# Kernel optimization log

Hardware: AMD Instinct MI355X
Metric: run time of the kernel (lower is better)

## Reference

```python
import jax, jax.numpy as jnp
import numpy as np

NB, HD, NL, NF = 5, 64, 4, 10           # num_bins, hidden_dim(d_model), num_layers, num_frames
DI, DS, DC, DTR = 128, 16, 4, 4          # d_inner=2*HD, d_state, d_conv, dt_rank=ceil(HD/16)
B, H, W = 4, 64, 64


def _conv2d(x, w, b):
    y = jax.lax.conv_general_dilated(x, w, (1, 1), 'SAME',
                                     dimension_numbers=('NCHW', 'OIHW', 'NCHW'))
    return y + b[None, :, None, None]


def _bn_relu(x, gamma, beta, eps=1e-5):
    # BatchNorm2d in training mode: biased batch stats over (N,H,W)
    mean = x.mean(axis=(0, 2, 3), keepdims=True)
    var = x.var(axis=(0, 2, 3), keepdims=True)
    y = (x - mean) * jax.lax.rsqrt(var + eps)
    return jax.nn.relu(y * gamma[None, :, None, None] + beta[None, :, None, None])


def _silu(x):
    return x * jax.nn.sigmoid(x)


def _causal_dwconv(x, w, b):
    # x: (B,L,DI), w: (DI,K) depthwise causal conv, b: (DI,)
    K = w.shape[1]
    L = x.shape[1]
    xp = jnp.pad(x, ((0, 0), (K - 1, 0), (0, 0)))
    y = sum(xp[:, k:k + L, :] * w[:, k] for k in range(K))
    return y + b


def _selective_scan(u, delta, A, Bm, Cm, D):
    # u,delta: (B,L,DI); A: (DI,DS); Bm,Cm: (B,L,DS); D: (DI,)
    dT, BT, CT, uT = (t.transpose(1, 0, 2) for t in (delta, Bm, Cm, u))
    h0 = jnp.zeros((u.shape[0], A.shape[0], A.shape[1]), u.dtype)

    def step(h, inp):
        d_t, B_t, C_t, u_t = inp                     # (B,DI),(B,DS),(B,DS),(B,DI)
        dA = jnp.exp(d_t[:, :, None] * A)            # (B,DI,DS)
        h = dA * h + (d_t * u_t)[:, :, None] * B_t[:, None, :]
        y = jnp.einsum('bds,bs->bd', h, C_t)
        return h, y

    _, ys = jax.lax.scan(step, h0, (dT, BT, CT, uT))  # ys: (L,B,DI)
    return ys.transpose(1, 0, 2) + u * D


def _mamba(x, in_proj, conv_w, conv_b, x_proj, dt_w, dt_b, A_log, Dp, out_proj):
    xz = x @ in_proj.T                               # (B,L,2*DI)
    xi, z = jnp.split(xz, 2, axis=-1)
    xi = _silu(_causal_dwconv(xi, conv_w, conv_b))
    xdbc = xi @ x_proj.T                             # (B,L,DTR+2*DS)
    dt, Bm, Cm = jnp.split(xdbc, [DTR, DTR + DS], axis=-1)
    delta = jax.nn.softplus(dt @ dt_w.T + dt_b)
    A = -jnp.exp(A_log)
    y = _selective_scan(xi, delta, A, Bm, Cm, Dp)
    return (y * _silu(z)) @ out_proj.T


def setup_inputs() -> dict:
    key = jax.random.key(0)
    ks = jax.random.split(key, 20)
    s = 0.02
    inp = {
        'x': jax.random.normal(ks[0], (B, NB, H, W), jnp.float32),
        'enc_w': jax.random.normal(ks[1], (HD, NB, 3, 3), jnp.float32) * s,
        'enc_b': jnp.zeros((HD,), jnp.float32),
        'enc_g': jnp.ones((HD,), jnp.float32),
        'enc_be': jnp.zeros((HD,), jnp.float32),
        'in_proj': jax.random.normal(ks[2], (NL, 2 * DI, HD), jnp.float32) * s,
        'conv_w': jax.random.normal(ks[3], (NL, DI, DC), jnp.float32) * s,
        'conv_b': jnp.zeros((NL, DI), jnp.float32),
        'x_proj': jax.random.normal(ks[4], (NL, DTR + 2 * DS, DI), jnp.float32) * s,
        'dt_w': jax.random.normal(ks[5], (NL, DI, DTR), jnp.float32) * s,
        'dt_b': jax.random.normal(ks[6], (NL, DI), jnp.float32) * 0.1 - 4.0,
        'A_log': jnp.broadcast_to(jnp.log(jnp.arange(1, DS + 1, dtype=jnp.float32)),
                                  (NL, DI, DS)).copy(),
        'Dp': jnp.ones((NL, DI), jnp.float32),
        'out_proj': jax.random.normal(ks[7], (NL, HD, DI), jnp.float32) * s,
        'dec1_w': jax.random.normal(ks[8], (HD, HD, 3, 3), jnp.float32) * s,
        'dec1_b': jnp.zeros((HD,), jnp.float32),
        'dec1_g': jnp.ones((HD,), jnp.float32),
        'dec1_be': jnp.zeros((HD,), jnp.float32),
        'dec2_w': jax.random.normal(ks[9], (NF, HD, 3, 3), jnp.float32) * s,
        'dec2_b': jnp.zeros((NF,), jnp.float32),
    }
    return inp


def reference(x, enc_w, enc_b, enc_g, enc_be, in_proj, conv_w, conv_b, x_proj,
              dt_w, dt_b, A_log, Dp, out_proj, dec1_w, dec1_b, dec1_g, dec1_be,
              dec2_w, dec2_b):
    Bb, _, Hh, Ww = x.shape
    h = _bn_relu(_conv2d(x, enc_w, enc_b), enc_g, enc_be)   # (B,HD,H,W)
    t = h.reshape(Bb, HD, Hh * Ww).transpose(0, 2, 1)        # (B,L,HD)
    for i in range(NL):
        t = t + _mamba(t, in_proj[i], conv_w[i], conv_b[i], x_proj[i],
                       dt_w[i], dt_b[i], A_log[i], Dp[i], out_proj[i])
    h = t.transpose(0, 2, 1).reshape(Bb, HD, Hh, Ww)
    h = _bn_relu(_conv2d(h, dec1_w, dec1_b), dec1_g, dec1_be)
    return _conv2d(h, dec2_w, dec2_b)                        # (B,NF,H,W)
```

## Files before the change

kernel.cpp:

```cpp
#include <hip/hip_runtime.h>
#include <hip/hip_bf16.h>

#define BB   4
#define NBC  5
#define HD   64
#define NLAYER 4
#define NFC  10
#define DIM  128
#define DSN  16
#define DCN  4
#define DTRK 4
#define HH   64
#define WWD  64
#define LL   4096
#define MM   (BB*LL)
#define NCHUNK 128
#define CLEN   32
#define TSTEP  16

__global__ void k_prep_all(const float* __restrict__ in_proj, const float* __restrict__ out_proj,
                           const float* __restrict__ dec1_w, const float* __restrict__ dec2_w,
                           float* __restrict__ wTin, float* __restrict__ wTout,
                           float* __restrict__ wT1, float* __restrict__ wT2,
                           float* __restrict__ stats, float* __restrict__ stats2) {
    int idx = blockIdx.x * blockDim.x + threadIdx.x;
    if (idx < 65536) {
        int n = idx & 255, k = (idx >> 8) & 63, l = idx >> 14;
        wTin[idx] = in_proj[(l << 14) + (n << 6) + k];
    } else if (idx < 98304) {
        int j = idx - 65536;
        int n = j & 63, k = (j >> 6) & 127, l = j >> 13;
        wTout[j] = out_proj[(l << 13) + (n << 7) + k];
    } else if (idx < 135168) {
        int j = idx - 98304;
        int co = j & 63, tap = (j >> 6) % 9, ci = j / 576;
        wT1[j] = dec1_w[co * 576 + ci * 9 + tap];
    } else if (idx < 142848) {
        int j = idx - 135168;
        int tap = j % 12, t2 = j / 12, co = t2 % NFC, ci = t2 / NFC;
        wT2[j] = (tap < 9) ? dec2_w[co * 576 + ci * 9 + tap] : 0.f;
    } else if (idx < 143104) {
        int j = idx - 142848;
        if (j < 128) stats[j] = 0.f; else stats2[j - 128] = 0.f;
    }
}

__global__ void k_enc_conv(const float* __restrict__ x, const float* __restrict__ w,
                           const float* __restrict__ bias, float* __restrict__ out,
                           float* __restrict__ stats) {
    __shared__ float r1[256], r2[256];
    int tid = threadIdx.x;
    int idx = blockIdx.x * 256 + tid;
    int wx = idx & 63;
    int hy = (idx >> 6) & 63;
    int co = (idx >> 12) & 63;
    int b  = idx >> 18;
    float acc = bias[co];
    for (int ci = 0; ci < NBC; ++ci) {
        const float* xin = x + (((long)(b * NBC + ci)) << 12);
        const float* wp  = w + (co * NBC + ci) * 9;
        #pragma unroll
        for (int kh = 0; kh < 3; ++kh) {
            int ih = hy + kh - 1;
            if (ih < 0 || ih >= HH) continue;
            #pragma unroll
            for (int kw = 0; kw < 3; ++kw) {
                int iw = wx + kw - 1;
                if (iw < 0 || iw >= WWD) continue;
                acc += xin[(ih << 6) + iw] * wp[kh * 3 + kw];
            }
        }
    }
    out[idx] = acc;
    r1[tid] = acc; r2[tid] = acc * acc;
    __syncthreads();
    for (int off = 128; off > 0; off >>= 1) {
        if (tid < off) { r1[tid] += r1[tid + off]; r2[tid] += r2[tid + off]; }
        __syncthreads();
    }
    if (tid == 0) {
        atomicAdd(&stats[co], r1[0]);
        atomicAdd(&stats[64 + co], r2[0]);
    }
}

__global__ __launch_bounds__(256, 1) void k_gemm_in_bn(const float* __restrict__ src,
                                                       const float* __restrict__ stats,
                                                       const float* __restrict__ g,
                                                       const float* __restrict__ be,
                                                       const float* __restrict__ wT,
                                                       float* __restrict__ tout,
                                                       float* __restrict__ xz) {
    __shared__ __align__(16) float ts[64 * 68];
    __shared__ float sc[64], sh[64];
    long m0 = (long)blockIdx.x << 6;
    int b = (int)(m0 >> 12);
    int hw0 = (int)(m0 & 4095);
    int tid = threadIdx.x;
    if (tid < 64) {
        float m = stats[tid] * (1.f / 16384.f);
        float var = stats[64 + tid] * (1.f / 16384.f) - m * m;
        float ss = g[tid] * rsqrtf(var + 1e-5f);
        sc[tid] = ss; sh[tid] = be[tid] - m * ss;
    }
    __syncthreads();
    for (int i = tid; i < 4096; i += 256) {
        int pix = i & 63, c = i >> 6;
        float v = src[(((long)((b << 6) + c)) << 12) + hw0 + pix];
        ts[pix * 68 + c] = fmaxf(v * sc[c] + sh[c], 0.f);
    }
    __syncthreads();
    for (int i = tid; i < 4096; i += 256) {
        int r = i >> 6, c = i & 63;
        tout[(m0 + r) * 64 + c] = ts[r * 68 + c];
    }
    int rg = tid >> 5;
    int cg = tid & 31;
    float acc[8][8] = {};
    int n0 = cg << 3;
    for (int k4 = 0; k4 < 16; ++k4) {
        float4 a[8];
        #pragma unroll
        for (int r2 = 0; r2 < 8; ++r2)
            a[r2] = *(const float4*)&ts[((rg << 3) + r2) * 68 + (k4 << 2)];
        #pragma unroll
        for (int kk = 0; kk < 4; ++kk) {
            const float* wr = wT + (((k4 << 2) + kk) << 8) + n0;
            float4 w0 = *(const float4*)&wr[0];
            float4 w1 = *(const float4*)&wr[4];
            #pragma unroll
            for (int r2 = 0; r2 < 8; ++r2) {
                float av = (kk == 0) ? a[r2].x : (kk == 1) ? a[r2].y
                         : (kk == 2) ? a[r2].z : a[r2].w;
                acc[r2][0] += av * w0.x; acc[r2][1] += av * w0.y;
                acc[r2][2] += av * w0.z; acc[r2][3] += av * w0.w;
                acc[r2][4] += av * w1.x; acc[r2][5] += av * w1.y;
                acc[r2][6] += av * w1.z; acc[r2][7] += av * w1.w;
            }
        }
    }
    #pragma unroll
    for (int r2 = 0; r2 < 8; ++r2) {
        long m = m0 + (rg << 3) + r2;
        *(float4*)&xz[(m << 8) + n0]     = make_float4(acc[r2][0], acc[r2][1], acc[r2][2], acc[r2][3]);
        *(float4*)&xz[(m << 8) + n0 + 4] = make_float4(acc[r2][4], acc[r2][5], acc[r2][6], acc[r2][7]);
    }
}

__global__ __launch_bounds__(256, 2) void k_xproj_fused(
        const float* __restrict__ xz, const float* __restrict__ cw,
        const float* __restrict__ cb, const float* __restrict__ Wx,
        const float* __restrict__ dw, const float* __restrict__ dbias,
        const float* __restrict__ A_log,
        float* __restrict__ xi, float* __restrict__ xdbc,
        float* __restrict__ delta, float* __restrict__ Pb, float* __restrict__ Sb) {
    __shared__ float xz_s[35 * 132];
    __shared__ float xi_s[32 * 132];
    __shared__ float w_s[36 * 132];
    __shared__ float xs[32 * 40];
    __shared__ float cwT[4 * 128];
    __shared__ float cb_s[128];
    long m0 = (long)blockIdx.x << 5;
    int l0 = (int)(m0 & 4095);
    int b = (int)(m0 >> 12);
    int chunk = l0 >> 5;
    int tid = threadIdx.x;

    for (int i = tid; i < 35 * 128; i += 256) {
        int j = i >> 7, k = i & 127;
        int l = l0 - 3 + j;
        float v = 0.f;
        if (l >= 0) v = xz[(m0 - 3 + j) * 256 + k];
        xz_s[j * 132 + k] = v;
    }
    if (tid < 128) cb_s[tid] = cb[tid];
    for (int i = tid; i < 512; i += 256) {
        int kk = i >> 7, di = i & 127;
        cwT[(kk << 7) + di] = cw[(di << 2) + kk];
    }
    for (int i = tid; i < 4608; i += 256) {
        int n = i >> 7, k = i & 127;
        w_s[n * 132 + k] = Wx[i];
    }
    __syncthreads();

    for (int ii = 0; ii < 4; ++ii) {
        int i = tid + (ii << 8);
        int r = i >> 5;
        int d4 = (i & 31) << 2;
        float4 a = *(const float4*)&cb_s[d4];
        #pragma unroll
        for (int kk = 0; kk < 4; ++kk) {
            float4 xv = *(const float4*)&xz_s[(r + kk) * 132 + d4];
            float4 wv = *(const float4*)&cwT[(kk << 7) + d4];
            a.x += xv.x * wv.x; a.y += xv.y * wv.y;
            a.z += xv.z * wv.z; a.w += xv.w * wv.w;
        }
        a.x = a.x / (1.f + __expf(-a.x));
        a.y = a.y / (1.f + __expf(-a.y));
        a.z = a.z / (1.f + __expf(-a.z));
        a.w = a.w / (1.f + __expf(-a.w));
        *(float4*)&xi_s[r * 132 + d4] = a;
        *(float4*)&xi[(m0 + r) * 128 + d4] = a;
    }
    __syncthreads();

    int n = tid & 63;
    int rg = tid >> 6;
    if (n < 36) {
        float acc[8] = {0,0,0,0,0,0,0,0};
        for (int k4 = 0; k4 < 32; ++k4) {
            float4 w4 = *(const float4*)&w_s[n * 132 + (k4 << 2)];
            #pragma unroll
            for (int r = 0; r < 8; ++r) {
                float4 a4 = *(const float4*)&xi_s[((rg << 3) + r) * 132 + (k4 << 2)];
                acc[r] += a4.x * w4.x + a4.y * w4.y + a4.z * w4.z + a4.w * w4.w;
            }
        }
        #pragma unroll
        for (int r = 0; r < 8; ++r) {
            int rr = (rg << 3) + r;
            xdbc[(m0 + rr) * 36 + n] = acc[r];
            xs[rr * 40 + n] = acc[r];
        }
    }
    __syncthreads();

    float* delta_s = xz_s;
    for (int i = tid; i < 4096; i += 256) {
        int r = i >> 7, di = i & 127;
        float v = dbias[di];
        float4 d4 = *(const float4*)&dw[di << 2];
        v += xs[r * 40 + 0] * d4.x + xs[r * 40 + 1] * d4.y
           + xs[r * 40 + 2] * d4.z + xs[r * 40 + 3] * d4.w;
        float sp = (v > 20.f) ? v : log1pf(expf(v));
        delta[(m0 + r) * 128 + di] = sp;
        delta_s[r * 132 + di] = sp;
    }
    __syncthreads();

    {
        int di = tid >> 1;
        int dso = (tid & 1) << 3;
        float4 al0 = *(const float4*)&A_log[(di << 4) + dso];
        float4 al1 = *(const float4*)&A_log[(di << 4) + dso + 4];
        float Av[8] = { -expf(al0.x), -expf(al0.y), -expf(al0.z), -expf(al0.w),
                        -expf(al1.x), -expf(al1.y), -expf(al1.z), -expf(al1.w) };
        float h[8] = {0,0,0,0,0,0,0,0};
        float P[8] = {1,1,1,1,1,1,1,1};
        #pragma unroll 4
        for (int i = 0; i < CLEN; ++i) {
            float d = delta_s[i * 132 + di];
            float u = xi_s[i * 132 + di];
            float du = d * u;
            float4 B0 = *(float4*)&xs[i * 40 + DTRK + dso];
            float4 B1 = *(float4*)&xs[i * 40 + DTRK + dso + 4];
            float a0 = __expf(d * Av[0]); h[0] = a0 * h[0] + du * B0.x; P[0] *= a0;
            float a1 = __expf(d * Av[1]); h[1] = a1 * h[1] + du * B0.y; P[1] *= a1;
            float a2 = __expf(d * Av[2]); h[2] = a2 * h[2] + du * B0.z; P[2] *= a2;
            float a3 = __expf(d * Av[3]); h[3] = a3 * h[3] + du * B0.w; P[3] *= a3;
            float a4 = __expf(d * Av[4]); h[4] = a4 * h[4] + du * B1.x; P[4] *= a4;
            float a5 = __expf(d * Av[5]); h[5] = a5 * h[5] + du * B1.y; P[5] *= a5;
            float a6 = __expf(d * Av[6]); h[6] = a6 * h[6] + du * B1.z; P[6] *= a6;
            float a7 = __expf(d * Av[7]); h[7] = a7 * h[7] + du * B1.w; P[7] *= a7;
        }
        long o = (((long)chunk * BB + b) << 11) + (di << 4) + dso;
        *(float4*)&Pb[o]     = make_float4(P[0], P[1], P[2], P[3]);
        *(float4*)&Pb[o + 4] = make_float4(P[4], P[5], P[6], P[7]);
        *(float4*)&Sb[o]     = make_float4(h[0], h[1], h[2], h[3]);
        *(float4*)&Sb[o + 4] = make_float4(h[4], h[5], h[6], h[7]);
    }
}

__global__ void k_scan_p2(float* Pb, const float* __restrict__ Sb) {
    int t = blockIdx.x * blockDim.x + threadIdx.x;
    int b = t >> 11;
    int s = t & 2047;
    float h = 0.f;
    for (int c = 0; c < NCHUNK; ++c) {
        long idx = (((long)c * BB + b) << 11) + s;
        float p = Pb[idx];
        float sv = Sb[idx];
        Pb[idx] = h;
        h = p * h + sv;
    }
}

__global__ __launch_bounds__(256, 1) void k_scan_p3_oi(
        const float* __restrict__ delta, const float* __restrict__ xi,
        const float* __restrict__ xdbc, const float* __restrict__ A_log,
        const float* __restrict__ Dp, const float* __restrict__ xz,
        const float* __restrict__ hin, const float* __restrict__ wTo,
        const float* __restrict__ wTi, float* __restrict__ tio,
        float* __restrict__ xz_out, int doB) {
    __shared__ __align__(16) float d_s[32 * 132];
    __shared__ __align__(16) float u_s[32 * 132];
    __shared__ __align__(16) float bc_s[32 * 36];
    __shared__ __align__(16) float t_s[32 * 68];
    int chunk = blockIdx.x, b = blockIdx.y;
    int tid = threadIdx.x;
    long t0 = ((long)b << 12) + (long)chunk * CLEN;

    for (int i = tid; i < 1024; i += 256) {
        int r = i >> 5, c4 = (i & 31) << 2;
        *(float4*)&d_s[r * 132 + c4] = *(const float4*)&delta[(t0 + r) * 128 + c4];
        *(float4*)&u_s[r * 132 + c4] = *(const float4*)&xi[(t0 + r) * 128 + c4];
    }
    {
        int r = tid >> 3, c4 = (tid & 7) << 2;
        *(float4*)&bc_s[r * 36 + c4] = *(const float4*)&xdbc[(t0 + r) * 36 + DTRK + c4];
    }

    int di = tid >> 1;
    int dso = (tid & 1) << 3;
    float4 al0 = *(const float4*)&A_log[(di << 4) + dso];
    float4 al1 = *(const float4*)&A_log[(di << 4) + dso + 4];
    float Av[8] = { -expf(al0.x), -expf(al0.y), -expf(al0.z), -expf(al0.w),
                    -expf(al1.x), -expf(al1.y), -expf(al1.z), -expf(al1.w) };
    float Dv = Dp[di];
    long o = (((long)chunk * BB + b) << 11) + (di << 4) + dso;
    float4 h0 = *(const float4*)&hin[o];
    float4 h1 = *(const float4*)&hin[o + 4];
    float h[8] = { h0.x, h0.y, h0.z, h0.w, h1.x, h1.y, h1.z, h1.w };
    __syncthreads();

    #pragma unroll 4
    for (int i = 0; i < CLEN; ++i) {
        float d = d_s[i * 132 + di];
        float u = u_s[i * 132 + di];
        float du = d * u;
        const float* bc = &bc_s[i * 36];
        float4 B0 = *(const float4*)&bc[dso];
        float4 B1 = *(const float4*)&bc[dso + 4];
        float4 C0 = *(const float4*)&bc[16 + dso];
        float4 C1 = *(const float4*)&bc[16 + dso + 4];
        float a0 = __expf(d * Av[0]); h[0] = a0 * h[0] + du * B0.x;
        float a1 = __expf(d * Av[1]); h[1] = a1 * h[1] + du * B0.y;
        float a2 = __expf(d * Av[2]); h[2] = a2 * h[2] + du * B0.z;
        float a3 = __expf(d * Av[3]); h[3] = a3 * h[3] + du * B0.w;
        float a4 = __expf(d * Av[4]); h[4] = a4 * h[4] + du * B1.x;
        float a5 = __expf(d * Av[5]); h[5] = a5 * h[5] + du * B1.y;
        float a6 = __expf(d * Av[6]); h[6] = a6 * h[6] + du * B1.z;
        float a7 = __expf(d * Av[7]); h[7] = a7 * h[7] + du * B1.w;
        float yp = h[0] * C0.x + h[1] * C0.y + h[2] * C0.z + h[3] * C0.w
                 + h[4] * C1.x + h[5] * C1.y + h[6] * C1.z + h[7] * C1.w;
        yp += __shfl_xor(yp, 1);
        if (dso == 0)
            u_s[i * 132 + di] = yp + u * Dv;
    }
    __syncthreads();

    for (int i = tid; i < 1024; i += 256) {
        int r = i >> 5, c4 = (i & 31) << 2;
        float4 y4 = *(float4*)&u_s[r * 132 + c4];
        float4 z4 = *(const float4*)&xz[((t0 + r) << 8) + DIM + c4];
        y4.x *= z4.x / (1.f + __expf(-z4.x));
        y4.y *= z4.y / (1.f + __expf(-z4.y));
        y4.z *= z4.z / (1.f + __expf(-z4.z));
        y4.w *= z4.w / (1.f + __expf(-z4.w));
        *(float4*)&u_s[r * 132 + c4] = y4;
    }
    __syncthreads();

    {
        int rg = tid >> 4, cg = tid & 15;
        int n0 = cg << 2;
        float acc[2][4] = {};
        for (int k4 = 0; k4 < 32; ++k4) {
            float4 a0 = *(const float4*)&u_s[(rg << 1) * 132 + (k4 << 2)];
            float4 a1 = *(const float4*)&u_s[((rg << 1) + 1) * 132 + (k4 << 2)];
            #pragma unroll
            for (int kk = 0; kk < 4; ++kk) {
                const float* wr = wTo + (((k4 << 2) + kk) << 6) + n0;
                float4 w0 = *(const float4*)&wr[0];
                float av0 = (kk == 0) ? a0.x : (kk == 1) ? a0.y : (kk == 2) ? a0.z : a0.w;
                float av1 = (kk == 0) ? a1.x : (kk == 1) ? a1.y : (kk == 2) ? a1.z : a1.w;
                acc[0][0] += av0 * w0.x; acc[0][1] += av0 * w0.y;
                acc[0][2] += av0 * w0.z; acc[0][3] += av0 * w0.w;
                acc[1][0] += av1 * w0.x; acc[1][1] += av1 * w0.y;
                acc[1][2] += av1 * w0.z; acc[1][3] += av1 * w0.w;
            }
        }
        #pragma unroll
        for (int r2 = 0; r2 < 2; ++r2) {
            long m = t0 + (rg << 1) + r2;
            float4 tv = *(const float4*)&tio[(m << 6) + n0];
            tv.x += acc[r2][0]; tv.y += acc[r2][1];
            tv.z += acc[r2][2]; tv.w += acc[r2][3];
            *(float4*)&tio[(m << 6) + n0] = tv;
            *(float4*)&t_s[((rg << 1) + r2) * 68 + n0] = tv;
        }
    }
    if (!doB) return;
    __syncthreads();

    {
        int rg = tid >> 5, cgn = tid & 31;
        int n0 = cgn << 3;
        float acc[4][8] = {};
        for (int k4 = 0; k4 < 16; ++k4) {
            float4 a[4];
            #pragma unroll
            for (int r2 = 0; r2 < 4; ++r2)
                a[r2] = *(const float4*)&t_s[((rg << 2) + r2) * 68 + (k4 << 2)];
            #pragma unroll
            for (int kk = 0; kk < 4; ++kk) {
                const float* wr = wTi + (((k4 << 2) + kk) << 8) + n0;
                float4 w0 = *(const float4*)&wr[0];
                float4 w1 = *(const float4*)&wr[4];
                #pragma unroll
                for (int r2 = 0; r2 < 4; ++r2) {
                    float av = (kk == 0) ? a[r2].x : (kk == 1) ? a[r2].y
                             : (kk == 2) ? a[r2].z : a[r2].w;
                    acc[r2][0] += av * w0.x; acc[r2][1] += av * w0.y;
                    acc[r2][2] += av * w0.z; acc[r2][3] += av * w0.w;
                    acc[r2][4] += av * w1.x; acc[r2][5] += av * w1.y;
                    acc[r2][6] += av * w1.z; acc[r2][7] += av * w1.w;
                }
            }
        }
        #pragma unroll
        for (int r2 = 0; r2 < 4; ++r2) {
            long m = t0 + (rg << 2) + r2;
            *(float4*)&xz_out[(m << 8) + n0]     = make_float4(acc[r2][0], acc[r2][1], acc[r2][2], acc[r2][3]);
            *(float4*)&xz_out[(m << 8) + n0 + 4] = make_float4(acc[r2][4], acc[r2][5], acc[r2][6], acc[r2][7]);
        }
    }
}

__global__ __launch_bounds__(256, 1) void k_dec1_new(const float* __restrict__ tin,
                                                     const float* __restrict__ wT,
                                                     const float* __restrict__ bias,
                                                     float* __restrict__ out,
                                                     float* __restrict__ stats2) {
    __shared__ __align__(16) float x_s[64 * 132];
    __shared__ __align__(16) float w_s[4 * 4608];
    int tile = blockIdx.x;
    int b = blockIdx.y;
    int ty0 = (tile >> 3) << 3;
    int tx0 = (tile & 7) << 3;
    int tid = threadIdx.x;
    int wv = tid >> 6;
    int lane = tid & 63;
    int r = lane >> 3;
    int cg = lane & 7;

    for (int i = tid; i < 6400; i += 256) {
        int pl = i >> 6;
        int c = i & 63;
        int py = pl / 10, px = pl - py * 10;
        int ih = ty0 + py - 1, iw = tx0 + px - 1;
        float v = 0.f;
        if (ih >= 0 && ih < HH && iw >= 0 && iw < WWD)
            v = tin[(((long)((b << 12) + (ih << 6) + iw)) << 6) + c];
        x_s[c * 132 + py * 12 + px] = v;
    }
    float* myw = &w_s[wv * 4608];
    const float* gw = wT + (wv * 16) * 576;
    float4 pref[18];
    #pragma unroll
    for (int i = 0; i < 18; ++i)
        pref[i] = *(const float4*)&gw[(i * 64 + lane) * 4];
    #pragma unroll
    for (int i = 0; i < 18; ++i)
        *(float4*)&myw[(i * 64 + lane) * 4] = pref[i];
    __syncthreads();

    float acc[8][8] = {};
    #pragma unroll
    for (int ch = 0; ch < 2; ++ch) {
        if (ch == 0) {
            const float* gw1 = wT + (wv * 16 + 8) * 576;
            #pragma unroll
            for (int i = 0; i < 18; ++i)
                pref[i] = *(const float4*)&gw1[(i * 64 + lane) * 4];
        }
        for (int cl = 0; cl < 8; ++cl) {
            int cib = wv * 16 + ch * 8 + cl;
            float xrow[3][10];
            #pragma unroll
            for (int kh = 0; kh < 3; ++kh) {
                const float* xr = &x_s[cib * 132 + (r + kh) * 12];
                float4 a0 = *(const float4*)&xr[0];
                float4 a1 = *(const float4*)&xr[4];
                float2 a2 = *(const float2*)&xr[8];
                xrow[kh][0] = a0.x; xrow[kh][1] = a0.y; xrow[kh][2] = a0.z; xrow[kh][3] = a0.w;
                xrow[kh][4] = a1.x; xrow[kh][5] = a1.y; xrow[kh][6] = a1.z; xrow[kh][7] = a1.w;
                xrow[kh][8] = a2.x; xrow[kh][9] = a2.y;
            }
            const float* wp = &myw[cl * 576];
            #pragma unroll
            for (int kh = 0; kh < 3; ++kh) {
                #pragma unroll
                for (int kw = 0; kw < 3; ++kw) {
                    const float* wp2 = wp + (kh * 3 + kw) * 64 + (cg << 3);
                    float4 wa = *(const float4*)&wp2[0];
                    float4 wb = *(const float4*)&wp2[4];
                    #pragma unroll
                    for (int j = 0; j < 8; ++j) {
                        float xv = xrow[kh][kw + j];
                        acc[j][0] += xv * wa.x; acc[j][1] += xv * wa.y;
                        acc[j][2] += xv * wa.z; acc[j][3] += xv * wa.w;
                        acc[j][4] += xv * wb.x; acc[j][5] += xv * wb.y;
                        acc[j][6] += xv * wb.z; acc[j][7] += xv * wb.w;
                    }
                }
            }
        }
        if (ch == 0) {
            #pragma unroll
            for (int i = 0; i < 18; ++i)
                *(float4*)&myw[(i * 64 + lane) * 4] = pref[i];
        }
    }

    #pragma unroll
    for (int j = 0; j < 8; ++j) {
        *(float4*)&myw[lane * 68 + (j << 3)]     = make_float4(acc[j][0], acc[j][1], acc[j][2], acc[j][3]);
        *(float4*)&myw[lane * 68 + (j << 3) + 4] = make_float4(acc[j][4], acc[j][5], acc[j][6], acc[j][7]);
    }
    __syncthreads();

    float bv = bias[lane];
    float ssum = 0.f, ssq = 0.f;
    #pragma unroll
    for (int pp = 0; pp < 16; ++pp) {
        int pr = (wv << 1) + (pp >> 3);
        int pc = pp & 7;
        int ol = (pr << 3) + (lane >> 3);
        int ix = (pc << 3) + (lane & 7);
        float s = w_s[ol * 68 + ix] + w_s[4608 + ol * 68 + ix]
                + w_s[9216 + ol * 68 + ix] + w_s[13824 + ol * 68 + ix] + bv;
        out[(((long)((b << 12) + ((ty0 + pr) << 6) + tx0 + pc)) << 6) + lane] = s;
        ssum += s; ssq += s * s;
    }
    float* red = x_s;
    red[(wv << 6) + lane] = ssum;
    red[256 + (wv << 6) + lane] = ssq;
    __syncthreads();
    if (tid < 64) {
        float a = red[tid] + red[64 + tid] + red[128 + tid] + red[192 + tid];
        float q = red[256 + tid] + red[320 + tid] + red[384 + tid] + red[448 + tid];
        atomicAdd(&stats2[tid], a);
        atomicAdd(&stats2[64 + tid], q);
    }
}

__global__ void k_dec2_fused(const float* __restrict__ src, const float* __restrict__ stats2,
                             const float* __restrict__ g, const float* __restrict__ be,
                             const float* __restrict__ wT, const float* __restrict__ bias,
                             float* __restrict__ out) {
    __shared__ float x_s[64 * 101];
    __shared__ float w_s[64 * NFC * 12];
    __shared__ float sc_s[64];
    __shared__ float sh_s[64];
    int tile = blockIdx.x;
    int b = blockIdx.y;
    int ty0 = (tile >> 3) << 3;
    int tx0 = (tile & 7) << 3;
    int tid = threadIdx.x;

    if (tid < 64) {
        float m = stats2[tid] * (1.f / 16384.f);
        float var = stats2[64 + tid] * (1.f / 16384.f) - m * m;
        float s = g[tid] * rsqrtf(var + 1e-5f);
        sc_s[tid] = s;
        sh_s[tid] = be[tid] - m * s;
    }
    for (int i = tid; i < 64 * NFC * 12; i += 256)
        w_s[i] = wT[i];
    __syncthreads();

    for (int i = tid; i < 6400; i += 256) {
        int pl = i >> 6;
        int c = i & 63;
        int py = pl / 10, px = pl - py * 10;
        int ih = ty0 + py - 1, iw = tx0 + px - 1;
        float v = 0.f;
        if (ih >= 0 && ih < HH && iw >= 0 && iw < WWD) {
            v = src[((long)((b << 12) + (ih << 6) + iw)) * 64 + c];
            v = fmaxf(v * sc_s[c] + sh_s[c], 0.f);
        }
        x_s[c * 101 + pl] = v;
    }
    __syncthreads();

    int px = tid & 63;
    int py = px >> 3, pxx = px & 7;
    int cog = tid >> 6;
    float acc[3] = {0.f, 0.f, 0.f};
    int nco = (cog < 2) ? 3 : 2;

    for (int ci = 0; ci < 64; ++ci) {
        const float* xr = &x_s[ci * 101 + py * 10 + pxx];
        float xv[9];
        #pragma unroll
        for (int kh = 0; kh < 3; ++kh)
            #pragma unroll
            for (int kw = 0; kw < 3; ++kw)
                xv[kh * 3 + kw] = xr[kh * 10 + kw];
        #pragma unroll
        for (int j = 0; j < 3; ++j) {
            if (j >= nco) break;
            int co = cog + (j << 2);
            const float* wp = &w_s[(ci * NFC + co) * 12];
            float4 w0 = *(const float4*)&wp[0];
            float4 w1 = *(const float4*)&wp[4];
            float  w8 = wp[8];
            acc[j] += xv[0] * w0.x + xv[1] * w0.y + xv[2] * w0.z + xv[3] * w0.w
                    + xv[4] * w1.x + xv[5] * w1.y + xv[6] * w1.z + xv[7] * w1.w
                    + xv[8] * w8;
        }
    }
    int hw = ((ty0 + py) << 6) + tx0 + pxx;
    #pragma unroll
    for (int j = 0; j < 3; ++j) {
        if (j >= nco) break;
        int co = cog + (j << 2);
        out[((long)(b * NFC + co) << 12) + hw] = acc[j] + bias[co];
    }
}

extern "C" void kernel_launch(void* const* d_in, const int* in_sizes, int n_in,
                              void* d_out, int out_size, void* d_ws, size_t ws_size,
                              hipStream_t stream) {
    const float* x       = (const float*)d_in[0];
    const float* enc_w   = (const float*)d_in[1];
    const float* enc_b   = (const float*)d_in[2];
    const float* enc_g   = (const float*)d_in[3];
    const float* enc_be  = (const float*)d_in[4];
    const float* in_proj = (const float*)d_in[5];
    const float* conv_w  = (const float*)d_in[6];
    const float* conv_b  = (const float*)d_in[7];
    const float* x_proj  = (const float*)d_in[8];
    const float* dt_w    = (const float*)d_in[9];
    const float* dt_b    = (const float*)d_in[10];
    const float* A_log   = (const float*)d_in[11];
    const float* Dp      = (const float*)d_in[12];
    const float* out_prj = (const float*)d_in[13];
    const float* dec1_w  = (const float*)d_in[14];
    const float* dec1_b  = (const float*)d_in[15];
    const float* dec1_g  = (const float*)d_in[16];
    const float* dec1_be = (const float*)d_in[17];
    const float* dec2_w  = (const float*)d_in[18];
    const float* dec2_b  = (const float*)d_in[19];
    float* out = (float*)d_out;

    float* ws = (float*)d_ws;
    size_t off = 0;
    float* conv_buf  = ws + off; off += 1048576;
    float* stats     = ws + off; off += 128;
    float* stats2    = ws + off; off += 128;
    float* wT1       = ws + off; off += 36864;
    float* wT2       = ws + off; off += 7680;
    float* wTin      = ws + off; off += 65536;
    float* wTout     = ws + off; off += 32768;
    float* t_buf     = ws + off; off += 1048576;
    float* xz_buf    = ws + off; off += 4194304;
    float* xi_buf    = ws + off; off += 2097152;
    float* xdbc_buf  = ws + off; off += 589824;
    float* delta_buf = ws + off; off += 2097152;
    float* Sb_buf    = ws + off; off += 1048576;
    (void)ws_size; (void)in_sizes; (void)n_in; (void)out_size;

    float* Pb = conv_buf;
    float* Sb = Sb_buf;

    k_prep_all<<<560, 256, 0, stream>>>(in_proj, out_prj, dec1_w, dec2_w,
                                        wTin, wTout, wT1, wT2, stats, stats2);

    k_enc_conv<<<4096, 256, 0, stream>>>(x, enc_w, enc_b, conv_buf, stats);

    k_gemm_in_bn<<<256, 256, 0, stream>>>(conv_buf, stats, enc_g, enc_be, wTin, t_buf, xz_buf);
    dim3 pg(NCHUNK, BB);
    for (int i = 0; i < NLAYER; ++i) {
        k_xproj_fused<<<512, 256, 0, stream>>>(xz_buf, conv_w + i * DIM * DCN,
                                               conv_b + i * DIM, x_proj + i * 36 * DIM,
                                               dt_w + i * DIM * DTRK, dt_b + i * DIM,
                                               A_log + i * DIM * DSN,
                                               xi_buf, xdbc_buf, delta_buf, Pb, Sb);
        k_scan_p2<<<32, 256, 0, stream>>>(Pb, Sb);
        int doB = (i < NLAYER - 1) ? 1 : 0;
        k_scan_p3_oi<<<pg, 256, 0, stream>>>(delta_buf, xi_buf, xdbc_buf,
                                             A_log + i * DIM * DSN, Dp + i * DIM,
                                             xz_buf, Pb, wTout + i * 8192,
                                             wTin + ((i + 1) & 3) * 16384,
                                             t_buf, xz_buf, doB);
    }

    dim3 dg1(64, BB);
    k_dec1_new<<<dg1, 256, 0, stream>>>(t_buf, wT1, dec1_b, conv_buf, stats2);
    k_dec2_fused<<<dg1, 256, 0, stream>>>(conv_buf, stats2, dec1_g, dec1_be, wT2, dec2_b, out);
}
```

Before: 489.8 us.

## Recompute delta in scan kernel instead of storing it to global memory

Stops writing the softplus delta tensor from the x-projection kernel and rebuilds it in the scan/out-proj kernel from the dt columns of xdbc. This removes a 2M-float global write and read per layer. The cost is extra exp/log1p work in the scan kernel. It also rebalances the x_proj mini-GEMM across 252 threads instead of 144 and aliases t_s onto d_s to cut LDS use.

```diff
diff --git a/kernel.cpp b/kernel.cpp
--- a/kernel.cpp
+++ b/kernel.cpp
@@ -16,7 +16,6 @@
 #define MM   (BB*LL)
 #define NCHUNK 128
 #define CLEN   32
-#define TSTEP  16
 
 __global__ void k_prep_all(const float* __restrict__ in_proj, const float* __restrict__ out_proj,
                            const float* __restrict__ dec1_w, const float* __restrict__ dec2_w,
@@ -153,7 +152,7 @@
         const float* __restrict__ dw, const float* __restrict__ dbias,
         const float* __restrict__ A_log,
         float* __restrict__ xi, float* __restrict__ xdbc,
-        float* __restrict__ delta, float* __restrict__ Pb, float* __restrict__ Sb) {
+        float* __restrict__ Pb, float* __restrict__ Sb) {
     __shared__ float xz_s[35 * 132];
     __shared__ float xi_s[32 * 132];
     __shared__ float w_s[36 * 132];
@@ -205,23 +204,31 @@
     }
     __syncthreads();
 
-    int n = tid & 63;
-    int rg = tid >> 6;
-    if (n < 36) {
-        float acc[8] = {0,0,0,0,0,0,0,0};
-        for (int k4 = 0; k4 < 32; ++k4) {
-            float4 w4 = *(const float4*)&w_s[n * 132 + (k4 << 2)];
-            #pragma unroll
-            for (int r = 0; r < 8; ++r) {
-                float4 a4 = *(const float4*)&xi_s[((rg << 3) + r) * 132 + (k4 << 2)];
-                acc[r] += a4.x * w4.x + a4.y * w4.y + a4.z * w4.z + a4.w * w4.w;
+    {
+        int g2 = tid / 36;
+        int n = tid - g2 * 36;
+        const int r0tab[8] = {0, 5, 10, 15, 20, 24, 28, 32};
+        if (g2 < 7) {
+            int rbeg = r0tab[g2];
+            int cnt = r0tab[g2 + 1] - rbeg;
+            float acc[5] = {0, 0, 0, 0, 0};
+            for (int k4 = 0; k4 < 32; ++k4) {
+                float4 w4 = *(const float4*)&w_s[n * 132 + (k4 << 2)];
+                #pragma unroll
+                for (int j = 0; j < 5; ++j) {
+                    int r = rbeg + j; r = (r > 31) ? 31 : r;
+                    float4 a4 = *(const float4*)&xi_s[r * 132 + (k4 << 2)];
+                    acc[j] += a4.x * w4.x + a4.y * w4.y + a4.z * w4.z + a4.w * w4.w;
+                }
             }
-        }
-        #pragma unroll
-        for (int r = 0; r < 8; ++r) {
-            int rr = (rg << 3) + r;
-            xdbc[(m0 + rr) * 36 + n] = acc[r];
-            xs[rr * 40 + n] = acc[r];
+            #pragma unroll
+            for (int j = 0; j < 5; ++j) {
+                if (j < cnt) {
+                    int r = rbeg + j;
+                    xdbc[(m0 + r) * 36 + n] = acc[j];
+                    xs[r * 40 + n] = acc[j];
+                }
+            }
         }
     }
     __syncthreads();
@@ -233,9 +240,7 @@
         float4 d4 = *(const float4*)&dw[di << 2];
         v += xs[r * 40 + 0] * d4.x + xs[r * 40 + 1] * d4.y
            + xs[r * 40 + 2] * d4.z + xs[r * 40 + 3] * d4.w;
-        float sp = (v > 20.f) ? v : log1pf(expf(v));
-        delta[(m0 + r) * 128 + di] = sp;
-        delta_s[r * 132 + di] = sp;
+        delta_s[r * 132 + di] = (v > 20.f) ? v : log1pf(expf(v));
     }
     __syncthreads();
 
@@ -287,28 +292,37 @@
 }
 
 __global__ __launch_bounds__(256, 1) void k_scan_p3_oi(
-        const float* __restrict__ delta, const float* __restrict__ xi,
-        const float* __restrict__ xdbc, const float* __restrict__ A_log,
+        const float* __restrict__ xi, const float* __restrict__ xdbc,
+        const float* __restrict__ A_log,
+        const float* __restrict__ dw, const float* __restrict__ dbias,
         const float* __restrict__ Dp, const float* __restrict__ xz,
         const float* __restrict__ hin, const float* __restrict__ wTo,
         const float* __restrict__ wTi, float* __restrict__ tio,
         float* __restrict__ xz_out, int doB) {
     __shared__ __align__(16) float d_s[32 * 132];
     __shared__ __align__(16) float u_s[32 * 132];
-    __shared__ __align__(16) float bc_s[32 * 36];
-    __shared__ __align__(16) float t_s[32 * 68];
+    __shared__ __align__(16) float bc_s[32 * 40];
     int chunk = blockIdx.x, b = blockIdx.y;
     int tid = threadIdx.x;
     long t0 = ((long)b << 12) + (long)chunk * CLEN;
 
     for (int i = tid; i < 1024; i += 256) {
         int r = i >> 5, c4 = (i & 31) << 2;
-        *(float4*)&d_s[r * 132 + c4] = *(const float4*)&delta[(t0 + r) * 128 + c4];
         *(float4*)&u_s[r * 132 + c4] = *(const float4*)&xi[(t0 + r) * 128 + c4];
     }
-    {
-        int r = tid >> 3, c4 = (tid & 7) << 2;
-        *(float4*)&bc_s[r * 36 + c4] = *(const float4*)&xdbc[(t0 + r) * 36 + DTRK + c4];
+    for (int i = tid; i < 288; i += 256) {
+        int r = i / 9, c4 = (i % 9) << 2;
+        *(float4*)&bc_s[r * 40 + c4] = *(const float4*)&xdbc[(t0 + r) * 36 + c4];
+    }
+    __syncthreads();
+
+    for (int i = tid; i < 4096; i += 256) {
+        int r = i >> 7, di = i & 127;
+        float v = dbias[di];
+        float4 d4 = *(const float4*)&dw[di << 2];
+        v += bc_s[r * 40 + 0] * d4.x + bc_s[r * 40 + 1] * d4.y
+           + bc_s[r * 40 + 2] * d4.z + bc_s[r * 40 + 3] * d4.w;
+        d_s[r * 132 + di] = (v > 20.f) ? v : log1pf(expf(v));
     }
 
     int di = tid >> 1;
@@ -329,11 +343,11 @@
         float d = d_s[i * 132 + di];
         float u = u_s[i * 132 + di];
         float du = d * u;
-        const float* bc = &bc_s[i * 36];
-        float4 B0 = *(const float4*)&bc[dso];
-        float4 B1 = *(const float4*)&bc[dso + 4];
-        float4 C0 = *(const float4*)&bc[16 + dso];
-        float4 C1 = *(const float4*)&bc[16 + dso + 4];
+        const float* bc = &bc_s[i * 40];
+        float4 B0 = *(const float4*)&bc[4 + dso];
+        float4 B1 = *(const float4*)&bc[8 + dso];
+        float4 C0 = *(const float4*)&bc[20 + dso];
+        float4 C1 = *(const float4*)&bc[24 + dso];
         float a0 = __expf(d * Av[0]); h[0] = a0 * h[0] + du * B0.x;
         float a1 = __expf(d * Av[1]); h[1] = a1 * h[1] + du * B0.y;
         float a2 = __expf(d * Av[2]); h[2] = a2 * h[2] + du * B0.z;
@@ -362,6 +376,7 @@
     }
     __syncthreads();
 
+    float* t_s = d_s;
     {
         int rg = tid >> 4, cg = tid & 15;
         int n0 = cg << 2;
@@ -659,7 +674,6 @@
     float* xz_buf    = ws + off; off += 4194304;
     float* xi_buf    = ws + off; off += 2097152;
     float* xdbc_buf  = ws + off; off += 589824;
-    float* delta_buf = ws + off; off += 2097152;
     float* Sb_buf    = ws + off; off += 1048576;
     (void)ws_size; (void)in_sizes; (void)n_in; (void)out_size;
 
@@ -678,11 +692,13 @@
                                                conv_b + i * DIM, x_proj + i * 36 * DIM,
                                                dt_w + i * DIM * DTRK, dt_b + i * DIM,
                                                A_log + i * DIM * DSN,
-                                               xi_buf, xdbc_buf, delta_buf, Pb, Sb);
+                                               xi_buf, xdbc_buf, Pb, Sb);
         k_scan_p2<<<32, 256, 0, stream>>>(Pb, Sb);
         int doB = (i < NLAYER - 1) ? 1 : 0;
-        k_scan_p3_oi<<<pg, 256, 0, stream>>>(delta_buf, xi_buf, xdbc_buf,
-                                             A_log + i * DIM * DSN, Dp + i * DIM,
+        k_scan_p3_oi<<<pg, 256, 0, stream>>>(xi_buf, xdbc_buf,
+                                             A_log + i * DIM * DSN,
+                                             dt_w + i * DIM * DTRK, dt_b + i * DIM,
+                                             Dp + i * DIM,
                                              xz_buf, Pb, wTout + i * 8192,
                                              wTin + ((i + 1) & 3) * 16384,
                                              t_buf, xz_buf, doB);
```

New measurement: 1.040 ms. +112.4%, slower.

## Halve scan chunk length to double chunk-level parallelism in scan phase three

Applied to the files above, without the earlier changes.

Changes the chunked selective scan from 128 chunks of 32 steps to 256 chunks of 16 steps. Phase one now emits two chunk summaries per block, and the fused phase-three kernel (scan plus out_proj and the next in_proj GEMM) now launches twice as many smaller blocks with less shared memory, aiming to fill the GPU better. In exchange the sequential phase-two pass over chunks doubles in length, the chunk buffers double in size and get their own workspace, and per-block GEMM reuse drops.

```diff
diff --git a/kernel.cpp b/kernel.cpp
--- a/kernel.cpp
+++ b/kernel.cpp
@@ -14,9 +14,8 @@
 #define WWD  64
 #define LL   4096
 #define MM   (BB*LL)
-#define NCHUNK 128
-#define CLEN   32
-#define TSTEP  16
+#define NCHUNK 256
+#define CLEN   16
 
 __global__ void k_prep_all(const float* __restrict__ in_proj, const float* __restrict__ out_proj,
                            const float* __restrict__ dec1_w, const float* __restrict__ dec2_w,
@@ -152,8 +151,8 @@
         const float* __restrict__ cb, const float* __restrict__ Wx,
         const float* __restrict__ dw, const float* __restrict__ dbias,
         const float* __restrict__ A_log,
-        float* __restrict__ xi, float* __restrict__ xdbc,
-        float* __restrict__ delta, float* __restrict__ Pb, float* __restrict__ Sb) {
+        float* __restrict__ xi, float* __restrict__ xdbc, float* __restrict__ delta,
+        float* __restrict__ Pb, float* __restrict__ Sb) {
     __shared__ float xz_s[35 * 132];
     __shared__ float xi_s[32 * 132];
     __shared__ float w_s[36 * 132];
@@ -163,7 +162,7 @@
     long m0 = (long)blockIdx.x << 5;
     int l0 = (int)(m0 & 4095);
     int b = (int)(m0 >> 12);
-    int chunk = l0 >> 5;
+    int chunk0 = l0 >> 4;
     int tid = threadIdx.x;
 
     for (int i = tid; i < 35 * 128; i += 256) {
@@ -246,29 +245,33 @@
         float4 al1 = *(const float4*)&A_log[(di << 4) + dso + 4];
         float Av[8] = { -expf(al0.x), -expf(al0.y), -expf(al0.z), -expf(al0.w),
                         -expf(al1.x), -expf(al1.y), -expf(al1.z), -expf(al1.w) };
-        float h[8] = {0,0,0,0,0,0,0,0};
-        float P[8] = {1,1,1,1,1,1,1,1};
-        #pragma unroll 4
-        for (int i = 0; i < CLEN; ++i) {
-            float d = delta_s[i * 132 + di];
-            float u = xi_s[i * 132 + di];
-            float du = d * u;
-            float4 B0 = *(float4*)&xs[i * 40 + DTRK + dso];
-            float4 B1 = *(float4*)&xs[i * 40 + DTRK + dso + 4];
-            float a0 = __expf(d * Av[0]); h[0] = a0 * h[0] + du * B0.x; P[0] *= a0;
-            float a1 = __expf(d * Av[1]); h[1] = a1 * h[1] + du * B0.y; P[1] *= a1;
-            float a2 = __expf(d * Av[2]); h[2] = a2 * h[2] + du * B0.z; P[2] *= a2;
-            float a3 = __expf(d * Av[3]); h[3] = a3 * h[3] + du * B0.w; P[3] *= a3;
-            float a4 = __expf(d * Av[4]); h[4] = a4 * h[4] + du * B1.x; P[4] *= a4;
-            float a5 = __expf(d * Av[5]); h[5] = a5 * h[5] + du * B1.y; P[5] *= a5;
-            float a6 = __expf(d * Av[6]); h[6] = a6 * h[6] + du * B1.z; P[6] *= a6;
-            float a7 = __expf(d * Av[7]); h[7] = a7 * h[7] + du * B1.w; P[7] *= a7;
-        }
-        long o = (((long)chunk * BB + b) << 11) + (di << 4) + dso;
-        *(float4*)&Pb[o]     = make_float4(P[0], P[1], P[2], P[3]);
-        *(float4*)&Pb[o + 4] = make_float4(P[4], P[5], P[6], P[7]);
-        *(float4*)&Sb[o]     = make_float4(h[0], h[1], h[2], h[3]);
-        *(float4*)&Sb[o + 4] = make_float4(h[4], h[5], h[6], h[7]);
+        #pragma unroll
+        for (int sub = 0; sub < 2; ++sub) {
+            float h[8] = {0,0,0,0,0,0,0,0};
+            float P[8] = {1,1,1,1,1,1,1,1};
+            #pragma unroll 4
+            for (int ii = 0; ii < CLEN; ++ii) {
+                int i = (sub << 4) + ii;
+                float d = delta_s[i * 132 + di];
+                float u = xi_s[i * 132 + di];
+                float du = d * u;
+                float4 B0 = *(float4*)&xs[i * 40 + DTRK + dso];
+                float4 B1 = *(float4*)&xs[i * 40 + DTRK + dso + 4];
+                float a0 = __expf(d * Av[0]); h[0] = a0 * h[0] + du * B0.x; P[0] *= a0;
+                float a1 = __expf(d * Av[1]); h[1] = a1 * h[1] + du * B0.y; P[1] *= a1;
+                float a2 = __expf(d * Av[2]); h[2] = a2 * h[2] + du * B0.z; P[2] *= a2;
+                float a3 = __expf(d * Av[3]); h[3] = a3 * h[3] + du * B0.w; P[3] *= a3;
+                float a4 = __expf(d * Av[4]); h[4] = a4 * h[4] + du * B1.x; P[4] *= a4;
+                float a5 = __expf(d * Av[5]); h[5] = a5 * h[5] + du * B1.y; P[5] *= a5;
+                float a6 = __expf(d * Av[6]); h[6] = a6 * h[6] + du * B1.z; P[6] *= a6;
+                float a7 = __expf(d * Av[7]); h[7] = a7 * h[7] + du * B1.w; P[7] *= a7;
+            }
+            long o = (((long)(chunk0 + sub) * BB + b) << 11) + (di << 4) + dso;
+            *(float4*)&Pb[o]     = make_float4(P[0], P[1], P[2], P[3]);
+            *(float4*)&Pb[o + 4] = make_float4(P[4], P[5], P[6], P[7]);
+            *(float4*)&Sb[o]     = make_float4(h[0], h[1], h[2], h[3]);
+            *(float4*)&Sb[o + 4] = make_float4(h[4], h[5], h[6], h[7]);
+        }
     }
 }
 
@@ -293,22 +296,21 @@
         const float* __restrict__ hin, const float* __restrict__ wTo,
         const float* __restrict__ wTi, float* __restrict__ tio,
         float* __restrict__ xz_out, int doB) {
-    __shared__ __align__(16) float d_s[32 * 132];
-    __shared__ __align__(16) float u_s[32 * 132];
-    __shared__ __align__(16) float bc_s[32 * 36];
-    __shared__ __align__(16) float t_s[32 * 68];
+    __shared__ __align__(16) float d_s[16 * 132];
+    __shared__ __align__(16) float u_s[16 * 132];
+    __shared__ __align__(16) float bc_s[16 * 40];
     int chunk = blockIdx.x, b = blockIdx.y;
     int tid = threadIdx.x;
     long t0 = ((long)b << 12) + (long)chunk * CLEN;
 
-    for (int i = tid; i < 1024; i += 256) {
+    for (int i = tid; i < 512; i += 256) {
         int r = i >> 5, c4 = (i & 31) << 2;
         *(float4*)&d_s[r * 132 + c4] = *(const float4*)&delta[(t0 + r) * 128 + c4];
         *(float4*)&u_s[r * 132 + c4] = *(const float4*)&xi[(t0 + r) * 128 + c4];
     }
-    {
-        int r = tid >> 3, c4 = (tid & 7) << 2;
-        *(float4*)&bc_s[r * 36 + c4] = *(const float4*)&xdbc[(t0 + r) * 36 + DTRK + c4];
+    if (tid < 144) {
+        int r = tid / 9, c4 = (tid % 9) << 2;
+        *(float4*)&bc_s[r * 40 + c4] = *(const float4*)&xdbc[(t0 + r) * 36 + c4];
     }
 
     int di = tid >> 1;
@@ -329,11 +331,11 @@
         float d = d_s[i * 132 + di];
         float u = u_s[i * 132 + di];
         float du = d * u;
-        const float* bc = &bc_s[i * 36];
-        float4 B0 = *(const float4*)&bc[dso];
-        float4 B1 = *(const float4*)&bc[dso + 4];
-        float4 C0 = *(const float4*)&bc[16 + dso];
-        float4 C1 = *(const float4*)&bc[16 + dso + 4];
+        const float* bc = &bc_s[i * 40];
+        float4 B0 = *(const float4*)&bc[4 + dso];
+        float4 B1 = *(const float4*)&bc[8 + dso];
+        float4 C0 = *(const float4*)&bc[20 + dso];
+        float4 C1 = *(const float4*)&bc[24 + dso];
         float a0 = __expf(d * Av[0]); h[0] = a0 * h[0] + du * B0.x;
         float a1 = __expf(d * Av[1]); h[1] = a1 * h[1] + du * B0.y;
         float a2 = __expf(d * Av[2]); h[2] = a2 * h[2] + du * B0.z;
@@ -350,7 +352,7 @@
     }
     __syncthreads();
 
-    for (int i = tid; i < 1024; i += 256) {
+    for (int i = tid; i < 512; i += 256) {
         int r = i >> 5, c4 = (i & 31) << 2;
         float4 y4 = *(float4*)&u_s[r * 132 + c4];
         float4 z4 = *(const float4*)&xz[((t0 + r) << 8) + DIM + c4];
@@ -362,66 +364,58 @@
     }
     __syncthreads();
 
+    float* t_s = d_s;
     {
-        int rg = tid >> 4, cg = tid & 15;
-        int n0 = cg << 2;
-        float acc[2][4] = {};
+        int r = tid >> 4;
+        int n0 = (tid & 15) << 2;
+        float acc[4] = {};
         for (int k4 = 0; k4 < 32; ++k4) {
-            float4 a0 = *(const float4*)&u_s[(rg << 1) * 132 + (k4 << 2)];
-            float4 a1 = *(const float4*)&u_s[((rg << 1) + 1) * 132 + (k4 << 2)];
+            float4 a = *(const float4*)&u_s[r * 132 + (k4 << 2)];
             #pragma unroll
             for (int kk = 0; kk < 4; ++kk) {
                 const float* wr = wTo + (((k4 << 2) + kk) << 6) + n0;
                 float4 w0 = *(const float4*)&wr[0];
+                float av = (kk == 0) ? a.x : (kk == 1) ? a.y : (kk == 2) ? a.z : a.w;
+                acc[0] += av * w0.x; acc[1] += av * w0.y;
+                acc[2] += av * w0.z; acc[3] += av * w0.w;
+            }
+        }
+        long m = t0 + r;
+        float4 tv = *(const float4*)&tio[(m << 6) + n0];
+        tv.x += acc[0]; tv.y += acc[1]; tv.z += acc[2]; tv.w += acc[3];
+        *(float4*)&tio[(m << 6) + n0] = tv;
+        *(float4*)&t_s[r * 68 + n0] = tv;
+    }
+    if (!doB) return;
+    __syncthreads();
+
+    {
+        int rg = tid >> 5;
+        int n0 = (tid & 31) << 3;
+        float acc[2][8] = {};
+        for (int k4 = 0; k4 < 16; ++k4) {
+            float4 a0 = *(const float4*)&t_s[(rg << 1) * 68 + (k4 << 2)];
+            float4 a1 = *(const float4*)&t_s[((rg << 1) + 1) * 68 + (k4 << 2)];
+            #pragma unroll
+            for (int kk = 0; kk < 4; ++kk) {
+                const float* wr = wTi + (((k4 << 2) + kk) << 8) + n0;
+                float4 w0 = *(const float4*)&wr[0];
+                float4 w1 = *(const float4*)&wr[4];
                 float av0 = (kk == 0) ? a0.x : (kk == 1) ? a0.y : (kk == 2) ? a0.z : a0.w;
                 float av1 = (kk == 0) ? a1.x : (kk == 1) ? a1.y : (kk == 2) ? a1.z : a1.w;
                 acc[0][0] += av0 * w0.x; acc[0][1] += av0 * w0.y;
                 acc[0][2] += av0 * w0.z; acc[0][3] += av0 * w0.w;
+                acc[0][4] += av0 * w1.x; acc[0][5] += av0 * w1.y;
+                acc[0][6] += av0 * w1.z; acc[0][7] += av0 * w1.w;
                 acc[1][0] += av1 * w0.x; acc[1][1] += av1 * w0.y;
                 acc[1][2] += av1 * w0.z; acc[1][3] += av1 * w0.w;
+                acc[1][4] += av1 * w1.x; acc[1][5] += av1 * w1.y;
+                acc[1][6] += av1 * w1.z; acc[1][7] += av1 * w1.w;
             }
         }
         #pragma unroll
         for (int r2 = 0; r2 < 2; ++r2) {
             long m = t0 + (rg << 1) + r2;
-            float4 tv = *(const float4*)&tio[(m << 6) + n0];
-            tv.x += acc[r2][0]; tv.y += acc[r2][1];
-            tv.z += acc[r2][2]; tv.w += acc[r2][3];
-            *(float4*)&tio[(m << 6) + n0] = tv;
-            *(float4*)&t_s[((rg << 1) + r2) * 68 + n0] = tv;
-        }
-    }
-    if (!doB) return;
-    __syncthreads();
-
-    {
-        int rg = tid >> 5, cgn = tid & 31;
-        int n0 = cgn << 3;
-        float acc[4][8] = {};
-        for (int k4 = 0; k4 < 16; ++k4) {
-            float4 a[4];
-            #pragma unroll
-            for (int r2 = 0; r2 < 4; ++r2)
-                a[r2] = *(const float4*)&t_s[((rg << 2) + r2) * 68 + (k4 << 2)];
-            #pragma unroll
-            for (int kk = 0; kk < 4; ++kk) {
-                const float* wr = wTi + (((k4 << 2) + kk) << 8) + n0;
-                float4 w0 = *(const float4*)&wr[0];
-                float4 w1 = *(const float4*)&wr[4];
-                #pragma unroll
-                for (int r2 = 0; r2 < 4; ++r2) {
-                    float av = (kk == 0) ? a[r2].x : (kk == 1) ? a[r2].y
-                             : (kk == 2) ? a[r2].z : a[r2].w;
-                    acc[r2][0] += av * w0.x; acc[r2][1] += av * w0.y;
-                    acc[r2][2] += av * w0.z; acc[r2][3] += av * w0.w;
-                    acc[r2][4] += av * w1.x; acc[r2][5] += av * w1.y;
-                    acc[r2][6] += av * w1.z; acc[r2][7] += av * w1.w;
-                }
-            }
-        }
-        #pragma unroll
-        for (int r2 = 0; r2 < 4; ++r2) {
-            long m = t0 + (rg << 2) + r2;
             *(float4*)&xz_out[(m << 8) + n0]     = make_float4(acc[r2][0], acc[r2][1], acc[r2][2], acc[r2][3]);
             *(float4*)&xz_out[(m << 8) + n0 + 4] = make_float4(acc[r2][4], acc[r2][5], acc[r2][6], acc[r2][7]);
         }
@@ -660,11 +654,9 @@
     float* xi_buf    = ws + off; off += 2097152;
     float* xdbc_buf  = ws + off; off += 589824;
     float* delta_buf = ws + off; off += 2097152;
-    float* Sb_buf    = ws + off; off += 1048576;
+    float* Pb_buf    = ws + off; off += 2097152;
+    float* Sb_buf    = ws + off; off += 2097152;
     (void)ws_size; (void)in_sizes; (void)n_in; (void)out_size;
-
-    float* Pb = conv_buf;
-    float* Sb = Sb_buf;
 
     k_prep_all<<<560, 256, 0, stream>>>(in_proj, out_prj, dec1_w, dec2_w,
                                         wTin, wTout, wT1, wT2, stats, stats2);
@@ -678,12 +670,12 @@
                                                conv_b + i * DIM, x_proj + i * 36 * DIM,
                                                dt_w + i * DIM * DTRK, dt_b + i * DIM,
                                                A_log + i * DIM * DSN,
-                                               xi_buf, xdbc_buf, delta_buf, Pb, Sb);
-        k_scan_p2<<<32, 256, 0, stream>>>(Pb, Sb);
+                                               xi_buf, xdbc_buf, delta_buf, Pb_buf, Sb_buf);
+        k_scan_p2<<<32, 256, 0, stream>>>(Pb_buf, Sb_buf);
         int doB = (i < NLAYER - 1) ? 1 : 0;
         k_scan_p3_oi<<<pg, 256, 0, stream>>>(delta_buf, xi_buf, xdbc_buf,
                                              A_log + i * DIM * DSN, Dp + i * DIM,
-                                             xz_buf, Pb, wTout + i * 8192,
+                                             xz_buf, Pb_buf, wTout + i * 8192,
                                              wTin + ((i + 1) & 3) * 16384,
                                              t_buf, xz_buf, doB);
     }
```

New measurement: 555.7 us. +13.5%, slower.
